# Kernel optimization log

Measured on AMD Instinct MI355X. Metric: run time of the kernel, lower is better.

Reference implementation:

```python
import jax, jax.numpy as jnp
import numpy as np

KTAPS = 10  # kernel_size in StructuredStateSpace.compute_cauchy_kernel


def setup_inputs() -> dict:
    key = jax.random.key(0)
    ks = jax.random.split(key, 6)
    T, B, F, L, OUT = 8192, 16, 32, 16, 128
    return {
        "x": jax.random.normal(ks[0], (T, B, F), dtype=jnp.float32),
        # K[l, s] = C_l @ A_l^s @ B_l, each an (F, F) matrix (in_features == hidden_size)
        "K": jax.random.normal(ks[1], (L, KTAPS, F, F), dtype=jnp.float32),
        # emission_layer[l]: nn.Linear(hidden_size, 1) -> weight (F,), bias scalar per l
        "em_w": jax.random.normal(ks[2], (L, F), dtype=jnp.float32),
        "em_b": jax.random.normal(ks[3], (L,), dtype=jnp.float32),
        # linear_decoder: nn.Linear(L, out_features)
        "dec_w": jax.random.normal(ks[4], (OUT, L), dtype=jnp.float32),
        "dec_b": jax.random.normal(ks[5], (OUT,), dtype=jnp.float32),
    }


def reference(x, K, em_w, em_b, dec_w, dec_b):
    # x: (T, B, F); K: (L, KTAPS, F, F)
    T, B, F = x.shape
    # causal conv: y[l, t] = sum_{s=0}^{min(t, KTAPS-1)} K[l, s] @ x[t - s]
    xp = jnp.pad(x, ((KTAPS - 1, 0), (0, 0), (0, 0)))  # (T+9, B, F)
    # X[s, t] = x[t - s]  -> (KTAPS, T, B, F); loop is over the fixed 10 taps only
    X = jnp.stack([xp[KTAPS - 1 - s:KTAPS - 1 - s + T] for s in range(KTAPS)], axis=0)
    y = jnp.einsum('lsof,stbf->ltbo', K, X)  # (L, T, B, F)
    # per-branch emission Linear(F, 1), stacked over L -> (T, B, L)
    h = jnp.einsum('ltbo,lo->tbl', y, em_w) + em_b
    h = jnp.swapaxes(h, 0, 1)  # (B, T, L)
    # linear_decoder: (B, T, L) -> (B, T, out_features)
    return h @ dec_w.T + dec_b
```

## Files before the change

### kernel.cpp

```cpp
#include <hip/hip_runtime.h>
#include <hip/hip_bf16.h>

typedef __attribute__((ext_vector_type(4))) float f32x4;
typedef __attribute__((ext_vector_type(8))) short bf16x8;

#define T_DIM 8192
#define B_DIM 16
#define F_DIM 32
#define L_DIM 16
#define NTAPS 10
#define O_DIM 128
#define M_TOTAL (T_DIM * B_DIM)
#define PADT (T_DIM + 16)

static __device__ __forceinline__ unsigned short f2bf(float f) {
    union { float f; unsigned int u; } v; v.f = f;
    unsigned int r = v.u + 0x7fffu + ((v.u >> 16) & 1u);
    return (unsigned short)(r >> 16);
}

__global__ __launch_bounds__(256) void build_w2_kernel(
    const float* __restrict__ K, const float* __restrict__ em_w,
    const float* __restrict__ em_b, const float* __restrict__ dec_w,
    const float* __restrict__ dec_b, unsigned short* __restrict__ w2f,
    float* __restrict__ bias2)
{
    int s = blockIdx.x;
    int tid = threadIdx.x;

    __shared__ float Klds[16 * 1024];
    __shared__ float Glds[16 * 32];

    #pragma unroll
    for (int l = 0; l < 16; ++l) {
        const float* src = K + (size_t)(l * NTAPS + s) * 1024 + tid * 4;
        *(f32x4*)(Klds + l * 1024 + tid * 4) = *(const f32x4*)src;
    }
    __syncthreads();

    #pragma unroll
    for (int rep = 0; rep < 2; ++rep) {
        int idx = rep * 256 + tid;
        int l = idx >> 5, f = idx & 31;
        const float* em = em_w + l * 32;
        const float* kb = Klds + l * 1024 + f;
        float g = 0.f;
        #pragma unroll
        for (int op = 0; op < 32; ++op) g += em[op] * kb[op * 32];
        Glds[idx] = g;
    }
    __syncthreads();

    int lane = tid & 63;
    int w    = tid >> 6;
    int lo   = lane & 15;
    int fb   = (lane >> 4) * 8;
    #pragma unroll
    for (int h = 0; h < 2; ++h) {
        int nt = w + h * 4;
        int o  = nt * 16 + lo;
        float acc[8] = {0.f,0.f,0.f,0.f,0.f,0.f,0.f,0.f};
        for (int l = 0; l < 16; ++l) {
            float dw = dec_w[o * L_DIM + l];
            const float* g = Glds + l * 32 + fb;
            #pragma unroll
            for (int j = 0; j < 8; ++j) acc[j] += dw * g[j];
        }
        unsigned short o8[8];
        #pragma unroll
        for (int j = 0; j < 8; ++j) o8[j] = f2bf(acc[j]);
        *(bf16x8*)(w2f + ((size_t)(s * 8 + nt) * 64 + lane) * 8) = *(const bf16x8*)o8;
    }

    if (s == 0 && tid < O_DIM) {
        float bsum = dec_b[tid];
        #pragma unroll
        for (int l = 0; l < 16; ++l) bsum += dec_w[tid * L_DIM + l] * em_b[l];
        bias2[tid] = bsum;
    }
}

__global__ __launch_bounds__(256) void convert_x_kernel(
    const float* __restrict__ x, unsigned short* __restrict__ xb)
{
    int b = blockIdx.y;
    int t = blockIdx.x * 256 + threadIdx.x;
    const float* src = x + ((size_t)t * B_DIM + b) * F_DIM;
    unsigned short* dst = xb + ((size_t)b * PADT + 16 + t) * F_DIM;
    #pragma unroll
    for (int c = 0; c < 4; ++c) {
        f32x4 a  = *(const f32x4*)(src + c * 8);
        f32x4 bb = *(const f32x4*)(src + c * 8 + 4);
        unsigned short r[8];
        #pragma unroll
        for (int j = 0; j < 4; ++j) { r[j] = f2bf(a[j]); r[4 + j] = f2bf(bb[j]); }
        *(bf16x8*)(dst + c * 8) = *(const bf16x8*)r;
    }
    if (blockIdx.x == 0 && threadIdx.x < 16) {
        unsigned short* pz = xb + ((size_t)b * PADT + threadIdx.x) * F_DIM;
        bf16x8 z = {0,0,0,0,0,0,0,0};
        #pragma unroll
        for (int c = 0; c < 4; ++c) *(bf16x8*)(pz + c * 8) = z;
    }
}

__global__ __launch_bounds__(256) void s4_main_kernel(
    const unsigned short* __restrict__ xb,
    const unsigned short* __restrict__ w2f,
    const float* __restrict__ bias2,
    float* __restrict__ out)
{
    int wave = threadIdx.x >> 6;
    int lane = threadIdx.x & 63;
    int R  = (blockIdx.x * 4 + wave) * 32;
    int b  = R >> 13;
    int t0 = R & (T_DIM - 1);
    size_t xrow = (size_t)b * PADT + 16 + t0;

    int lo = lane & 15;
    int fb = (lane >> 4) * 8;

    f32x4 acc[2][8];
    #pragma unroll
    for (int mt = 0; mt < 2; ++mt)
        #pragma unroll
        for (int nt = 0; nt < 8; ++nt)
            acc[mt][nt] = (f32x4){0.f, 0.f, 0.f, 0.f};

    for (int s = 0; s < NTAPS; ++s) {
        bf16x8 wfrag[8];
        const bf16x8* wp = (const bf16x8*)w2f + (size_t)s * 8 * 64 + lane;
        #pragma unroll
        for (int nt = 0; nt < 8; ++nt) wfrag[nt] = wp[nt * 64];

        #pragma unroll
        for (int mt = 0; mt < 2; ++mt) {
            bf16x8 xfrag = *(const bf16x8*)(xb + (xrow + mt * 16 + lo - s) * F_DIM + fb);
            #pragma unroll
            for (int nt = 0; nt < 8; ++nt)
                acc[mt][nt] = __builtin_amdgcn_mfma_f32_16x16x32_bf16(
                    wfrag[nt], xfrag, acc[mt][nt], 0, 0, 0);
        }
    }

    int q = lane >> 4;
    #pragma unroll
    for (int nt = 0; nt < 8; ++nt) {
        f32x4 bi = *(const f32x4*)(bias2 + nt * 16 + q * 4);
        #pragma unroll
        for (int mt = 0; mt < 2; ++mt) {
            size_t r = (size_t)R + mt * 16 + lo;
            f32x4 v = acc[mt][nt] + bi;
            *(f32x4*)(out + r * O_DIM + nt * 16 + q * 4) = v;
        }
    }
}

extern "C" void kernel_launch(void* const* d_in, const int* in_sizes, int n_in,
                              void* d_out, int out_size, void* d_ws, size_t ws_size,
                              hipStream_t stream)
{
    const float* x     = (const float*)d_in[0];
    const float* K     = (const float*)d_in[1];
    const float* em_w  = (const float*)d_in[2];
    const float* em_b  = (const float*)d_in[3];
    const float* dec_w = (const float*)d_in[4];
    const float* dec_b = (const float*)d_in[5];
    float* out = (float*)d_out;

    const size_t xb_bytes  = (size_t)B_DIM * PADT * F_DIM * 2;
    const size_t w2f_bytes = (size_t)NTAPS * 8 * 64 * 8 * 2;
    unsigned short* xb  = (unsigned short*)d_ws;
    unsigned short* w2f = (unsigned short*)((char*)d_ws + xb_bytes);
    float* bias2 = (float*)((char*)d_ws + xb_bytes + w2f_bytes);

    hipLaunchKernelGGL(build_w2_kernel, dim3(NTAPS), dim3(256), 0, stream,
                       K, em_w, em_b, dec_w, dec_b, w2f, bias2);
    hipLaunchKernelGGL(convert_x_kernel, dim3(T_DIM / 256, B_DIM), dim3(256), 0, stream,
                       x, xb);
    hipLaunchKernelGGL(s4_main_kernel, dim3(M_TOTAL / 128), dim3(256), 0, stream,
                       xb, w2f, bias2, out);
}
```

Baseline: 122.3 us.

## Fuse x bf16 conversion into main kernel via LDS staging; parallelize weight prep

Drops the separate x-to-bf16 conversion kernel and its padded global buffer. The main kernel now loads fp32 x directly, converts it and stages a 272-row halo tile in LDS, and all 10 taps read shifted rows from there. Blocks grow to 512 threads covering 256 rows, and bias is loaded before the MFMA loop. The single-block-per-tap weight-build kernel is split into two more parallel kernels (G reduction, then W2 build) spread over many more blocks, at the cost of one extra launch.

```diff
diff --git a/kernel.cpp b/kernel.cpp
--- a/kernel.cpp
+++ b/kernel.cpp
@@ -3,6 +3,7 @@
 
 typedef __attribute__((ext_vector_type(4))) float f32x4;
 typedef __attribute__((ext_vector_type(8))) short bf16x8;
+typedef __attribute__((ext_vector_type(4))) short bf16x4;
 
 #define T_DIM 8192
 #define B_DIM 16
@@ -11,7 +12,10 @@
 #define NTAPS 10
 #define O_DIM 128
 #define M_TOTAL (T_DIM * B_DIM)
-#define PADT (T_DIM + 16)
+
+#define G_OFF    0
+#define W2F_OFF  20480
+#define BIAS_OFF 102400
 
 static __device__ __forceinline__ unsigned short f2bf(float f) {
     union { float f; unsigned int u; } v; v.f = f;
@@ -19,106 +23,108 @@
     return (unsigned short)(r >> 16);
 }
 
-__global__ __launch_bounds__(256) void build_w2_kernel(
+__global__ __launch_bounds__(256) void g_stage_kernel(
     const float* __restrict__ K, const float* __restrict__ em_w,
-    const float* __restrict__ em_b, const float* __restrict__ dec_w,
-    const float* __restrict__ dec_b, unsigned short* __restrict__ w2f,
-    float* __restrict__ bias2)
+    float* __restrict__ G)
 {
-    int s = blockIdx.x;
-    int tid = threadIdx.x;
-
-    __shared__ float Klds[16 * 1024];
-    __shared__ float Glds[16 * 32];
-
+    int s = blockIdx.x >> 4, l = blockIdx.x & 15;
+    int f = threadIdx.x & 31, opg = threadIdx.x >> 5;
+    const float* Kb = K + (size_t)(l * NTAPS + s) * 1024;
+    float p = 0.f;
     #pragma unroll
-    for (int l = 0; l < 16; ++l) {
-        const float* src = K + (size_t)(l * NTAPS + s) * 1024 + tid * 4;
-        *(f32x4*)(Klds + l * 1024 + tid * 4) = *(const f32x4*)src;
+    for (int k = 0; k < 4; ++k) {
+        int op = opg * 4 + k;
+        p += em_w[l * 32 + op] * Kb[op * 32 + f];
     }
+    __shared__ float red[8][32];
+    red[opg][f] = p;
     __syncthreads();
-
-    #pragma unroll
-    for (int rep = 0; rep < 2; ++rep) {
-        int idx = rep * 256 + tid;
-        int l = idx >> 5, f = idx & 31;
-        const float* em = em_w + l * 32;
-        const float* kb = Klds + l * 1024 + f;
+    if (threadIdx.x < 32) {
         float g = 0.f;
         #pragma unroll
-        for (int op = 0; op < 32; ++op) g += em[op] * kb[op * 32];
-        Glds[idx] = g;
-    }
-    __syncthreads();
-
-    int lane = tid & 63;
-    int w    = tid >> 6;
-    int lo   = lane & 15;
-    int fb   = (lane >> 4) * 8;
-    #pragma unroll
-    for (int h = 0; h < 2; ++h) {
-        int nt = w + h * 4;
-        int o  = nt * 16 + lo;
-        float acc[8] = {0.f,0.f,0.f,0.f,0.f,0.f,0.f,0.f};
-        for (int l = 0; l < 16; ++l) {
-            float dw = dec_w[o * L_DIM + l];
-            const float* g = Glds + l * 32 + fb;
-            #pragma unroll
-            for (int j = 0; j < 8; ++j) acc[j] += dw * g[j];
-        }
-        unsigned short o8[8];
-        #pragma unroll
-        for (int j = 0; j < 8; ++j) o8[j] = f2bf(acc[j]);
-        *(bf16x8*)(w2f + ((size_t)(s * 8 + nt) * 64 + lane) * 8) = *(const bf16x8*)o8;
-    }
-
-    if (s == 0 && tid < O_DIM) {
-        float bsum = dec_b[tid];
-        #pragma unroll
-        for (int l = 0; l < 16; ++l) bsum += dec_w[tid * L_DIM + l] * em_b[l];
-        bias2[tid] = bsum;
+        for (int q = 0; q < 8; ++q) g += red[q][threadIdx.x];
+        G[(s * 16 + l) * 32 + threadIdx.x] = g;
     }
 }
 
-__global__ __launch_bounds__(256) void convert_x_kernel(
-    const float* __restrict__ x, unsigned short* __restrict__ xb)
+__global__ __launch_bounds__(256) void build_w2_kernel(
+    const float* __restrict__ G, const float* __restrict__ em_b,
+    const float* __restrict__ dec_w, const float* __restrict__ dec_b,
+    unsigned short* __restrict__ w2f, float* __restrict__ bias2)
 {
-    int b = blockIdx.y;
-    int t = blockIdx.x * 256 + threadIdx.x;
-    const float* src = x + ((size_t)t * B_DIM + b) * F_DIM;
-    unsigned short* dst = xb + ((size_t)b * PADT + 16 + t) * F_DIM;
+    int s = blockIdx.x >> 3, nt = blockIdx.x & 7;
+    int lane = threadIdx.x & 63, w = threadIdx.x >> 6;
+    int lo = lane & 15, fb = (lane >> 4) * 8;
+    int o = nt * 16 + lo;
+
+    float acc[8] = {0.f,0.f,0.f,0.f,0.f,0.f,0.f,0.f};
     #pragma unroll
-    for (int c = 0; c < 4; ++c) {
-        f32x4 a  = *(const f32x4*)(src + c * 8);
-        f32x4 bb = *(const f32x4*)(src + c * 8 + 4);
-        unsigned short r[8];
+    for (int l = 0; l < 4; ++l) {
+        int ll = w * 4 + l;
+        float dw = dec_w[o * L_DIM + ll];
+        const float* g = G + (s * 16 + ll) * 32 + fb;
         #pragma unroll
-        for (int j = 0; j < 4; ++j) { r[j] = f2bf(a[j]); r[4 + j] = f2bf(bb[j]); }
-        *(bf16x8*)(dst + c * 8) = *(const bf16x8*)r;
+        for (int j = 0; j < 8; ++j) acc[j] += dw * g[j];
     }
-    if (blockIdx.x == 0 && threadIdx.x < 16) {
-        unsigned short* pz = xb + ((size_t)b * PADT + threadIdx.x) * F_DIM;
-        bf16x8 z = {0,0,0,0,0,0,0,0};
+    __shared__ float red[4][64][8];
+    #pragma unroll
+    for (int j = 0; j < 8; ++j) red[w][lane][j] = acc[j];
+    __syncthreads();
+    if (w == 0) {
+        unsigned short o8[8];
         #pragma unroll
-        for (int c = 0; c < 4; ++c) *(bf16x8*)(pz + c * 8) = z;
+        for (int j = 0; j < 8; ++j)
+            o8[j] = f2bf(red[0][lane][j] + red[1][lane][j] +
+                         red[2][lane][j] + red[3][lane][j]);
+        *(bf16x8*)(w2f + ((size_t)(s * 8 + nt) * 64 + lane) * 8) = *(const bf16x8*)o8;
+    }
+    if (s == 0 && nt == 0 && threadIdx.x < O_DIM) {
+        float b = dec_b[threadIdx.x];
+        #pragma unroll
+        for (int l = 0; l < 16; ++l) b += dec_w[threadIdx.x * L_DIM + l] * em_b[l];
+        bias2[threadIdx.x] = b;
     }
 }
 
-__global__ __launch_bounds__(256) void s4_main_kernel(
-    const unsigned short* __restrict__ xb,
-    const unsigned short* __restrict__ w2f,
-    const float* __restrict__ bias2,
-    float* __restrict__ out)
+#define XROWS 272
+#define XSTRIDE 80
+
+__global__ __launch_bounds__(512) void s4_main_kernel(
+    const float* __restrict__ x, const unsigned short* __restrict__ w2f,
+    const float* __restrict__ bias2, float* __restrict__ out)
 {
-    int wave = threadIdx.x >> 6;
-    int lane = threadIdx.x & 63;
-    int R  = (blockIdx.x * 4 + wave) * 32;
-    int b  = R >> 13;
-    int t0 = R & (T_DIM - 1);
-    size_t xrow = (size_t)b * PADT + 16 + t0;
+    __shared__ char xlds[XROWS * XSTRIDE];
 
-    int lo = lane & 15;
-    int fb = (lane >> 4) * 8;
+    int tid  = threadIdx.x;
+    int lane = tid & 63, w = tid >> 6;
+    int lo = lane & 15, g = lane >> 4;
+
+    int Rb = blockIdx.x * 256;
+    int b  = Rb >> 13;
+    int t0 = Rb & (T_DIM - 1);
+
+    #pragma unroll
+    for (int rep = 0; rep < 5; ++rep) {
+        int c = rep * 512 + tid;
+        if (c < XROWS * 8) {
+            int i = c >> 3, part = c & 7;
+            int t = t0 + i - 16;
+            unsigned short r4[4] = {0, 0, 0, 0};
+            if (t >= 0) {
+                f32x4 v = *(const f32x4*)(x + ((size_t)t * B_DIM + b) * F_DIM + part * 4);
+                #pragma unroll
+                for (int j = 0; j < 4; ++j) r4[j] = f2bf(v[j]);
+            }
+            *(bf16x4*)(xlds + i * XSTRIDE + part * 8) = *(const bf16x4*)r4;
+        }
+    }
+
+    f32x4 bias[8];
+    #pragma unroll
+    for (int nt = 0; nt < 8; ++nt)
+        bias[nt] = *(const f32x4*)(bias2 + nt * 16 + g * 4);
+
+    __syncthreads();
 
     f32x4 acc[2][8];
     #pragma unroll
@@ -127,31 +133,29 @@
         for (int nt = 0; nt < 8; ++nt)
             acc[mt][nt] = (f32x4){0.f, 0.f, 0.f, 0.f};
 
+    int ib = 16 + w * 32 + lo;
     for (int s = 0; s < NTAPS; ++s) {
-        bf16x8 wfrag[8];
+        bf16x8 wf[8];
         const bf16x8* wp = (const bf16x8*)w2f + (size_t)s * 8 * 64 + lane;
         #pragma unroll
-        for (int nt = 0; nt < 8; ++nt) wfrag[nt] = wp[nt * 64];
-
+        for (int nt = 0; nt < 8; ++nt) wf[nt] = wp[nt * 64];
         #pragma unroll
         for (int mt = 0; mt < 2; ++mt) {
-            bf16x8 xfrag = *(const bf16x8*)(xb + (xrow + mt * 16 + lo - s) * F_DIM + fb);
+            bf16x8 xf = *(const bf16x8*)(xlds + (ib + mt * 16 - s) * XSTRIDE + g * 16);
             #pragma unroll
             for (int nt = 0; nt < 8; ++nt)
                 acc[mt][nt] = __builtin_amdgcn_mfma_f32_16x16x32_bf16(
-                    wfrag[nt], xfrag, acc[mt][nt], 0, 0, 0);
+                    wf[nt], xf, acc[mt][nt], 0, 0, 0);
         }
     }
 
-    int q = lane >> 4;
     #pragma unroll
     for (int nt = 0; nt < 8; ++nt) {
-        f32x4 bi = *(const f32x4*)(bias2 + nt * 16 + q * 4);
         #pragma unroll
         for (int mt = 0; mt < 2; ++mt) {
-            size_t r = (size_t)R + mt * 16 + lo;
-            f32x4 v = acc[mt][nt] + bi;
-            *(f32x4*)(out + r * O_DIM + nt * 16 + q * 4) = v;
+            size_t r = (size_t)Rb + w * 32 + mt * 16 + lo;
+            f32x4 v = acc[mt][nt] + bias[nt];
+            *(f32x4*)(out + r * O_DIM + nt * 16 + g * 4) = v;
         }
     }
 }
@@ -168,16 +172,14 @@
     const float* dec_b = (const float*)d_in[5];
     float* out = (float*)d_out;
 
-    const size_t xb_bytes  = (size_t)B_DIM * PADT * F_DIM * 2;
-    const size_t w2f_bytes = (size_t)NTAPS * 8 * 64 * 8 * 2;
-    unsigned short* xb  = (unsigned short*)d_ws;
-    unsigned short* w2f = (unsigned short*)((char*)d_ws + xb_bytes);
-    float* bias2 = (float*)((char*)d_ws + xb_bytes + w2f_bytes);
+    float*          Gbuf  = (float*)((char*)d_ws + G_OFF);
+    unsigned short* w2f   = (unsigned short*)((char*)d_ws + W2F_OFF);
+    float*          bias2 = (float*)((char*)d_ws + BIAS_OFF);
 
-    hipLaunchKernelGGL(build_w2_kernel, dim3(NTAPS), dim3(256), 0, stream,
-                       K, em_w, em_b, dec_w, dec_b, w2f, bias2);
-    hipLaunchKernelGGL(convert_x_kernel, dim3(T_DIM / 256, B_DIM), dim3(256), 0, stream,
-                       x, xb);
-    hipLaunchKernelGGL(s4_main_kernel, dim3(M_TOTAL / 128), dim3(256), 0, stream,
-                       xb, w2f, bias2, out);
+    hipLaunchKernelGGL(g_stage_kernel, dim3(NTAPS * 16), dim3(256), 0, stream,
+                       K, em_w, Gbuf);
+    hipLaunchKernelGGL(build_w2_kernel, dim3(NTAPS * 8), dim3(256), 0, stream,
+                       Gbuf, em_b, dec_w, dec_b, w2f, bias2);
+    hipLaunchKernelGGL(s4_main_kernel, dim3(M_TOTAL / 256), dim3(512), 0, stream,
+                       x, w2f, bias2, out);
 }
```

Measured after the change: 110.0 us. -10.0%, faster.
